# Optimization experiments

Measured on AMD Instinct MI355X. Metric: run time of the kernel, lower is better.

## Reference

```python
import jax, jax.numpy as jnp
import numpy as np

B, STATE_DIM, MLP_DIM, H, W = 128, 64, 512, 40, 40
LN_EPS = 1e-5


def _sobel_kernel(c):
    # Per-channel depthwise filters in torch order: [c0_sx, c0_sy, c0_id, c1_sx, ...]
    sx = jnp.array([[-1., 0., 1.], [-2., 0., 2.], [-1., 0., 1.]], jnp.float32)
    sy = jnp.array([[-1., -2., -1.], [0., 0., 0.], [1., 2., 1.]], jnp.float32)
    ident = jnp.array([[0., 0., 0.], [0., 1., 0.], [0., 0., 0.]], jnp.float32)
    k = jnp.stack([sx, sy, ident])[:, None]      # [3, 1, 3, 3]
    return jnp.tile(k, (c, 1, 1, 1))             # [3c, 1, 3, 3]


def setup_inputs() -> dict:
    key = jax.random.key(0)
    ks = jax.random.split(key, 6)
    state_in = jax.random.normal(ks[0], (B, STATE_DIM, H, W), jnp.float32)
    w1 = jax.random.normal(ks[1], (MLP_DIM, 3 * STATE_DIM), jnp.float32) * 0.05
    ln_weight = jax.random.uniform(ks[2], (MLP_DIM, H, W), jnp.float32, 0.5, 1.5)
    ln_bias = jax.random.normal(ks[3], (MLP_DIM, H, W), jnp.float32) * 0.01
    w2 = jax.random.normal(ks[4], (STATE_DIM, MLP_DIM), jnp.float32) * 0.05
    mask = jax.random.randint(ks[5], (H, W), 0, 2, jnp.int32)  # bernoulli(0.5) update mask
    return {"state_in": state_in, "w1": w1, "ln_weight": ln_weight,
            "ln_bias": ln_bias, "w2": w2, "mask": mask}


def reference(state_in, w1, ln_weight, ln_bias, w2, mask):
    C = state_in.shape[1]
    # Depthwise 3x3 sobel/identity perception: [B, C, H, W] -> [B, 3C, H, W]
    kern = _sobel_kernel(C)
    x = jax.lax.conv_general_dilated(
        state_in, kern, window_strides=(1, 1), padding='SAME',
        dimension_numbers=('NCHW', 'OIHW', 'NCHW'), feature_group_count=C)
    # 1x1 conv (no bias): [B, 3C, H, W] -> [B, MLP, H, W]
    x = jnp.einsum('bchw,oc->bohw', x, w1)
    # LayerNorm over (MLP, H, W) per sample, with elementwise affine
    mu = jnp.mean(x, axis=(1, 2, 3), keepdims=True)
    var = jnp.var(x, axis=(1, 2, 3), keepdims=True)
    x = (x - mu) * jax.lax.rsqrt(var + LN_EPS) * ln_weight + ln_bias
    x = jax.nn.relu(x)
    # 1x1 conv back to state channels (zero-init in original; random here for testing)
    x = jnp.einsum('bchw,oc->bohw', x, w2)
    # Stochastic per-pixel update mask, broadcast over batch and channels
    x = x * mask.astype(jnp.float32)
    # Alive mask: 3x3 max-pool on alive channel, stride 1, SAME padding
    live = jax.lax.reduce_window(state_in[:, 3], -jnp.inf, jax.lax.max,
                                 (1, 3, 3), (1, 1, 1), 'SAME')
    live = (live > 0.1).astype(jnp.float32)[:, None]  # [B, 1, H, W]
    return state_in + x * live
```

## Files before the change

### kernel.cpp

```cpp
#include <hip/hip_runtime.h>


typedef unsigned short u16;
typedef unsigned int   u32;
typedef __attribute__((ext_vector_type(8))) u16    ushort8;
typedef __attribute__((ext_vector_type(4))) u16    u16x4;
typedef __attribute__((ext_vector_type(8))) __bf16 bf16x8;
typedef __attribute__((ext_vector_type(4))) float  f32x4;
typedef __attribute__((ext_vector_type(4))) u32    u32x4;

#define NB   128
#define NC   64
#define K1   192
#define NO   512
#define NHW  1600
#define LN_N 819200.0f

__device__ __forceinline__ u16 f2bf(float f) {
    union { float f; u32 u; } v; v.f = f;
    u32 u = v.u;
    u32 r = u + 0x7fffu + ((u >> 16) & 1u);
    return (u16)(r >> 16);
}
__device__ __forceinline__ float bf2f(u16 h) {
    union { u32 u; float f; } v; v.u = ((u32)h) << 16; return v.f;
}
__device__ __forceinline__ f32x4 mfma16(bf16x8 a, bf16x8 b, f32x4 c) {
    return __builtin_amdgcn_mfma_f32_16x16x32_bf16(a, b, c, 0, 0, 0);
}
__device__ __forceinline__ bf16x8 ldfrag(const u16* p) {
    return *(const bf16x8*)p;
}

__device__ __forceinline__ void load_halo(const float* __restrict__ base, int h,
                                          int wq, float reg[3][12]) {
#pragma unroll
    for (int jj = 0; jj < 3; ++jj) {
        int hh = h + jj - 1;
        bool vh = (unsigned)hh < 40u;
        const float* rowp = base + hh * 40;
#pragma unroll
        for (int i = 0; i < 12; ++i) {
            int col = wq * 10 - 1 + i;
            reg[jj][i] = (vh && (unsigned)col < 40u) ? rowp[col] : 0.0f;
        }
    }
}
__device__ __forceinline__ void sobel_px(const float reg[3][12], int t,
                                         float& sx, float& sy, float& idn) {
    sx = (reg[0][t + 2] - reg[0][t]) + 2.0f * (reg[1][t + 2] - reg[1][t])
       + (reg[2][t + 2] - reg[2][t]);
    sy = (reg[2][t] + 2.0f * reg[2][t + 1] + reg[2][t + 2])
       - (reg[0][t] + 2.0f * reg[0][t + 1] + reg[0][t + 2]);
    idn = reg[1][t + 1];
}

__global__ __launch_bounds__(256) void k0_convert(const float* __restrict__ w1,
                                                  const float* __restrict__ w2,
                                                  u16* __restrict__ w1b,
                                                  u16* __restrict__ w1T,
                                                  u16* __restrict__ w2b,
                                                  float* __restrict__ stats) {
    int g = blockIdx.x * 256 + threadIdx.x;
    if (g < NO * K1) {
        u16 v = f2bf(w1[g]);
        w1b[g] = v;
        int o = g / K1, k = g - o * K1;
        w1T[(size_t)k * NO + o] = v;
    } else if (g < NO * K1 + NC * NO) {
        w2b[g - NO * K1] = f2bf(w2[g - NO * K1]);
    } else if (g < NO * K1 + NC * NO + 256) {
        stats[g - NO * K1 - NC * NO] = 0.0f;
    }
}

__global__ __launch_bounds__(256) void k0_lncomb(const float* __restrict__ lnw,
                                                 const float* __restrict__ lnb,
                                                 u32* __restrict__ lncT) {
    __shared__ u32 t[32][33];
    int p0 = blockIdx.x * 32, o0 = blockIdx.y * 32;
    int tx = threadIdx.x & 31, ty = threadIdx.x >> 5;
#pragma unroll
    for (int k = 0; k < 4; ++k) {
        size_t gi = (size_t)(o0 + ty + k * 8) * NHW + p0 + tx;
        t[ty + k * 8][tx] = ((u32)f2bf(lnb[gi]) << 16) | f2bf(lnw[gi]);
    }
    __syncthreads();
#pragma unroll
    for (int k = 0; k < 4; ++k)
        lncT[(size_t)(p0 + ty + k * 8) * NO + o0 + tx] = t[tx][ty + k * 8];
}

__global__ __launch_bounds__(256) void k0_gram(const u16* __restrict__ w1T,
                                               float* __restrict__ G,
                                               float* __restrict__ colw1) {
    const int blk = blockIdx.x;
    const int tid = threadIdx.x;
    const int lane = tid & 63, wid = tid >> 6;
    const int q = lane >> 4, l15 = lane & 15;
    if (blk < 36) {
        int bj = blk / 6, bk = blk - bj * 6;
        int j0 = bj * 32 + (wid & 1) * 16, k0 = bk * 32 + (wid >> 1) * 16;
        f32x4 acc = {0.f, 0.f, 0.f, 0.f};
#pragma unroll
        for (int ks = 0; ks < 16; ++ks) {
            bf16x8 a  = ldfrag(&w1T[(size_t)(j0 + l15) * NO + ks * 32 + q * 8]);
            bf16x8 bb = ldfrag(&w1T[(size_t)(k0 + l15) * NO + ks * 32 + q * 8]);
            acc = mfma16(a, bb, acc);
        }
#pragma unroll
        for (int r = 0; r < 4; ++r)
            G[(size_t)(j0 + q * 4 + r) * K1 + k0 + l15] = acc[r];
    } else if (tid < K1) {
        float s = 0.f;
        for (int i = 0; i < NO / 8; ++i) {
            ushort8 v = *(const ushort8*)&w1T[(size_t)tid * NO + i * 8];
#pragma unroll
            for (int j = 0; j < 8; ++j) s += bf2f(v[j]);
        }
        colw1[tid] = s;
    }
}

__global__ __launch_bounds__(256) void k2_stats(const float* __restrict__ state,
                                                const float* __restrict__ G,
                                                const float* __restrict__ colw1,
                                                float* __restrict__ stats) {
    const int b = blockIdx.x >> 2, quarter = blockIdx.x & 3;
    const int tid = threadIdx.x;
    const int lane = tid & 63, wid = tid >> 6;
    const int q = lane >> 4, l15 = lane & 15;
    const int j0 = (wid & 1) * 96, j1 = (wid >> 1) * 96, jo = wid * 48;

    __shared__ __align__(16) u16 Pt[208 * 104];
    __shared__ float red[8];

    for (int i = tid; i < 208 * 104 / 2; i += 256) ((u32*)Pt)[i] = 0u;
    __syncthreads();
    if (tid < 80) Pt[192 * 104 + tid] = 0x3F80u;

    f32x4 acc[6][6], accO[3];
#pragma unroll
    for (int i = 0; i < 6; ++i)
#pragma unroll
        for (int j = 0; j < 6; ++j) { f32x4 z = {0.f,0.f,0.f,0.f}; acc[i][j] = z; }
#pragma unroll
    for (int j = 0; j < 3; ++j) { f32x4 z = {0.f,0.f,0.f,0.f}; accO[j] = z; }

    const int c = tid >> 2, wq = tid & 3;
    const float* base = state + ((size_t)b * NC + c) * NHW;

    for (int tile = 0; tile < 5; ++tile) {
        const int h0 = (quarter * 5 + tile) * 2;
        __syncthreads();
        for (int rr = 0; rr < 2; ++rr) {
            float reg[3][12];
            load_halo(base, h0 + rr, wq, reg);
#pragma unroll
            for (int t = 0; t < 10; ++t) {
                float sx, sy, idn; sobel_px(reg, t, sx, sy, idn);
                int px = rr * 40 + wq * 10 + t;
                Pt[(3 * c + 0) * 104 + px] = f2bf(sx);
                Pt[(3 * c + 1) * 104 + px] = f2bf(sy);
                Pt[(3 * c + 2) * 104 + px] = f2bf(idn);
            }
        }
        __syncthreads();
#pragma unroll
        for (int ks = 0; ks < 3; ++ks) {
            bf16x8 av[6], bv[6], ao, bo[3];
#pragma unroll
            for (int fi = 0; fi < 6; ++fi)
                av[fi] = ldfrag(&Pt[(j0 + fi * 16 + l15) * 104 + ks * 32 + q * 8]);
#pragma unroll
            for (int fj = 0; fj < 6; ++fj)
                bv[fj] = ldfrag(&Pt[(j1 + fj * 16 + l15) * 104 + ks * 32 + q * 8]);
            ao = ldfrag(&Pt[(192 + l15) * 104 + ks * 32 + q * 8]);
#pragma unroll
            for (int fj = 0; fj < 3; ++fj)
                bo[fj] = ldfrag(&Pt[(jo + fj * 16 + l15) * 104 + ks * 32 + q * 8]);
#pragma unroll
            for (int fi = 0; fi < 6; ++fi)
#pragma unroll
                for (int fj = 0; fj < 6; ++fj)
                    acc[fi][fj] = mfma16(av[fi], bv[fj], acc[fi][fj]);
#pragma unroll
            for (int fj = 0; fj < 3; ++fj)
                accO[fj] = mfma16(ao, bo[fj], accO[fj]);
        }
    }

    float ssq = 0.f;
#pragma unroll
    for (int fi = 0; fi < 6; ++fi)
#pragma unroll
        for (int fj = 0; fj < 6; ++fj) {
            f32x4 gv = *(const f32x4*)&G[(size_t)(j1 + fj * 16 + l15) * K1
                                         + j0 + fi * 16 + q * 4];
#pragma unroll
            for (int r = 0; r < 4; ++r) ssq += acc[fi][fj][r] * gv[r];
        }
    float sm = 0.f;
    if (q == 0) {
#pragma unroll
        for (int fj = 0; fj < 3; ++fj)
            sm += accO[fj][0] * colw1[jo + fj * 16 + l15];
    }
#pragma unroll
    for (int off = 32; off > 0; off >>= 1) {
        ssq += __shfl_down(ssq, off);
        sm  += __shfl_down(sm, off);
    }
    if (lane == 0) { red[wid] = ssq; red[4 + wid] = sm; }
    __syncthreads();
    if (tid == 0) {
        atomicAdd(&stats[b * 2],     red[4] + red[5] + red[6] + red[7]);
        atomicAdd(&stats[b * 2 + 1], red[0] + red[1] + red[2] + red[3]);
    }
}

__global__ void k3_finalize(const float* __restrict__ stats, float2* __restrict__ musig) {
    int t = threadIdx.x;
    if (t < NB) {
        float s = stats[2 * t], qq = stats[2 * t + 1];
        float inv = 1.0f / LN_N;
        float mu = s * inv;
        float var = qq * inv - mu * mu;
        float2 r; r.x = mu; r.y = rsqrtf(var + 1e-5f);
        musig[t] = r;
    }
}

__global__ __launch_bounds__(256, 3) void k4_fused(const float* __restrict__ state,
                                                   const u16* __restrict__ w1b,
                                                   const u16* __restrict__ w2b,
                                                   const u32* __restrict__ lncT,
                                                   const int* __restrict__ mask,
                                                   const float2* __restrict__ musig,
                                                   float* __restrict__ out) {
    const int bx = blockIdx.x;
    const int b  = blockIdx.y;
    const int p0 = bx * 80, h0 = bx * 2;
    const int tid = threadIdx.x;
    const int lane = tid & 63, wid = tid >> 6;
    const int q = lane >> 4, l15 = lane & 15;

    __shared__ __align__(16) u16 Pt[80 * 192];
    __shared__ __align__(16) u16 Ys[80 * 128];
    __shared__ __align__(16) float gate[80];

    const float2 ms = musig[b];
    const float mu = ms.x, rs = ms.y;

    {
        const int c = tid >> 2, wq = tid & 3;
        const float* base = state + ((size_t)b * NC + c) * NHW;
        for (int rr = 0; rr < 2; ++rr) {
            float reg[3][12];
            load_halo(base, h0 + rr, wq, reg);
#pragma unroll
            for (int t = 0; t < 10; ++t) {
                float sx, sy, idn; sobel_px(reg, t, sx, sy, idn);
                int px = rr * 40 + wq * 10 + t;
                int k = 3 * c;
#pragma unroll
                for (int i = 0; i < 3; ++i) {
                    int kk = k + i, u = kk >> 3;
                    int elem = px * 192 + (((u & 0x18) | ((u ^ px) & 7)) << 3) + (kk & 7);
                    Pt[elem] = f2bf(i == 0 ? sx : (i == 1 ? sy : idn));
                }
            }
        }
    }
    if (tid < 80) {
        int p = p0 + tid;
        int h = p / 40, w = p - h * 40;
        const float* st3 = state + ((size_t)b * NC + 3) * NHW;
        float mx = -1e30f;
#pragma unroll
        for (int dh = -1; dh <= 1; ++dh) {
            int hh = h + dh;
            if ((unsigned)hh < 40u)
#pragma unroll
                for (int dw = -1; dw <= 1; ++dw) {
                    int wc = w + dw;
                    if ((unsigned)wc < 40u) mx = fmaxf(mx, st3[hh * 40 + wc]);
                }
        }
        gate[tid] = (mx > 0.1f && mask[p] != 0) ? 1.0f : 0.0f;
    }
    __syncthreads();

    float g5[5];
#pragma unroll
    for (int mi = 0; mi < 5; ++mi) g5[mi] = gate[mi * 16 + l15];

    f32x4 acc2[5];
#pragma unroll
    for (int i = 0; i < 5; ++i) { f32x4 z = {0.f,0.f,0.f,0.f}; acc2[i] = z; }

    const int ogw = wid * 32;

    for (int oc = 0; oc < 4; ++oc) {
        const int ob = oc * 128 + ogw;
        f32x4 acc1[2][5];
#pragma unroll
        for (int f = 0; f < 2; ++f)
#pragma unroll
            for (int i = 0; i < 5; ++i) { f32x4 z = {0.f,0.f,0.f,0.f}; acc1[f][i] = z; }
#pragma unroll
        for (int ks = 0; ks < 6; ++ks) {
            bf16x8 a0 = ldfrag(&w1b[(size_t)(ob + l15) * K1 + ks * 32 + q * 8]);
            bf16x8 a1 = ldfrag(&w1b[(size_t)(ob + 16 + l15) * K1 + ks * 32 + q * 8]);
#pragma unroll
            for (int mi = 0; mi < 5; ++mi) {
                int r = mi * 16 + l15, u = ks * 4 + q;
                bf16x8 bp = ldfrag(&Pt[r * 192 + (((u & 0x18) | ((u ^ r) & 7)) << 3)]);
                acc1[0][mi] = mfma16(a0, bp, acc1[0][mi]);
                acc1[1][mi] = mfma16(a1, bp, acc1[1][mi]);
            }
        }
#pragma unroll
        for (int f = 0; f < 2; ++f) {
#pragma unroll
            for (int mi = 0; mi < 5; ++mi) {
                int p = mi * 16 + l15;
                int oglob = ob + f * 16 + q * 4;
                u32x4 lv = *(const u32x4*)&lncT[(size_t)(p0 + p) * NO + oglob];
                u16x4 yv;
#pragma unroll
                for (int r = 0; r < 4; ++r) {
                    float lw = bf2f((u16)(lv[r] & 0xffffu));
                    float lb = bf2f((u16)(lv[r] >> 16));
                    float y = (acc1[f][mi][r] - mu) * rs * lw + lb;
                    yv[r] = f2bf(fmaxf(y, 0.0f));
                }
                int u = wid * 4 + f * 2 + (q >> 1);
                int up = u ^ (p & 7);
                *(u16x4*)&Ys[p * 128 + up * 8 + (q & 1) * 4] = yv;
            }
        }
        __syncthreads();
#pragma unroll
        for (int ks2 = 0; ks2 < 4; ++ks2) {
            bf16x8 aw = ldfrag(&w2b[(size_t)(wid * 16 + l15) * NO
                                    + oc * 128 + ks2 * 32 + q * 8]);
#pragma unroll
            for (int mi = 0; mi < 5; ++mi) {
                int p = mi * 16 + l15;
                int u = ks2 * 4 + q;
                int up = u ^ (p & 7);
                bf16x8 by = ldfrag(&Ys[p * 128 + up * 8]);
                acc2[mi] = mfma16(aw, by, acc2[mi]);
            }
        }
        __syncthreads();
    }

#pragma unroll
    for (int mi = 0; mi < 5; ++mi) {
        int p = p0 + mi * 16 + l15;
        float g = g5[mi];
#pragma unroll
        for (int r = 0; r < 4; ++r) {
            int s = wid * 16 + q * 4 + r;
            size_t idx = ((size_t)b * NC + s) * NHW + p;
            out[idx] = state[idx] + g * acc2[mi][r];
        }
    }
}

extern "C" void kernel_launch(void* const* d_in, const int* in_sizes, int n_in,
                              void* d_out, int out_size, void* d_ws, size_t ws_size,
                              hipStream_t stream) {
    const float* state = (const float*)d_in[0];
    const float* w1    = (const float*)d_in[1];
    const float* lnw   = (const float*)d_in[2];
    const float* lnb   = (const float*)d_in[3];
    const float* w2    = (const float*)d_in[4];
    const int*   mask  = (const int*)d_in[5];
    float* out = (float*)d_out;

    char* ws = (char*)d_ws;
    u16*    w1b   = (u16*)(ws + 0ull);
    u16*    w2b   = (u16*)(ws + 196608ull);
    u32*    lncT  = (u32*)(ws + 262144ull);
    u16*    w1T   = (u16*)(ws + 3538944ull);
    float*  G     = (float*)(ws + 3735552ull);
    float*  colw1 = (float*)(ws + 3883008ull);
    float*  stats = (float*)(ws + 3883776ull);
    float2* musig = (float2*)(ws + 3884800ull);

    k0_convert <<<513, 256, 0, stream>>>(w1, w2, w1b, w1T, w2b, stats);
    k0_lncomb  <<<dim3(50, 16), 256, 0, stream>>>(lnw, lnb, lncT);
    k0_gram    <<<37, 256, 0, stream>>>(w1T, G, colw1);
    k2_stats   <<<512, 256, 0, stream>>>(state, G, colw1, stats);
    k3_finalize<<<1, 128, 0, stream>>>(stats, musig);
    k4_fused   <<<dim3(20, 128), 256, 0, stream>>>(state, w1b, w2b, lncT,
                                                   mask, musig, out);
}
```

Before: 337.7 us.

## Prepack weights and LN params in MFMA fragment order, shrink per-iteration tile

Weights w1/w2 and the combined LN weight/bias are rearranged in the setup kernels into the exact per-lane fragment order the fused kernel consumes, so each wave loads them with contiguous vector reads. The output-channel loop now runs 8 chunks of 64 instead of 4 of 128, which halves the accumulator set and the Ys shared buffer so that 4 blocks per CU can be requested. The alive/mask gate is computed per lane in registers instead of through shared memory, and the LN affine is folded into FMAs. The cost is more iterations, which means more barriers per block, plus duplicated max-pool reads in every wave.

```diff
diff --git a/kernel.cpp b/kernel.cpp
--- a/kernel.cpp
+++ b/kernel.cpp
@@ -25,6 +25,12 @@
 __device__ __forceinline__ float bf2f(u16 h) {
     union { u32 u; float f; } v; v.u = ((u32)h) << 16; return v.f;
 }
+__device__ __forceinline__ float bfhi(u32 c) {
+    union { u32 u; float f; } v; v.u = c & 0xffff0000u; return v.f;
+}
+__device__ __forceinline__ float bflo(u32 c) {
+    union { u32 u; float f; } v; v.u = c << 16; return v.f;
+}
 __device__ __forceinline__ f32x4 mfma16(bf16x8 a, bf16x8 b, f32x4 c) {
     return __builtin_amdgcn_mfma_f32_16x16x32_bf16(a, b, c, 0, 0, 0);
 }
@@ -57,18 +63,25 @@
 
 __global__ __launch_bounds__(256) void k0_convert(const float* __restrict__ w1,
                                                   const float* __restrict__ w2,
-                                                  u16* __restrict__ w1b,
+                                                  u16* __restrict__ w1p,
                                                   u16* __restrict__ w1T,
-                                                  u16* __restrict__ w2b,
+                                                  u16* __restrict__ w2p,
                                                   float* __restrict__ stats) {
     int g = blockIdx.x * 256 + threadIdx.x;
     if (g < NO * K1) {
         u16 v = f2bf(w1[g]);
-        w1b[g] = v;
         int o = g / K1, k = g - o * K1;
+        int f = o >> 4, ks = k >> 5;
+        int lane = (((k >> 3) & 3) << 4) | (o & 15);
+        w1p[(size_t)(((f * 6 + ks) * 64 + lane) * 8 + (k & 7))] = v;
         w1T[(size_t)k * NO + o] = v;
     } else if (g < NO * K1 + NC * NO) {
-        w2b[g - NO * K1] = f2bf(w2[g - NO * K1]);
+        int i = g - NO * K1;
+        int s = i / NO, o = i - s * NO;
+        u16 v = f2bf(w2[i]);
+        int wid = s >> 4, oc = o >> 6, ks2 = (o >> 5) & 1;
+        int lane = (((o >> 3) & 3) << 4) | (s & 15);
+        w2p[(size_t)((((wid * 8 + oc) * 2 + ks2) * 64 + lane) * 8 + (o & 7))] = v;
     } else if (g < NO * K1 + NC * NO + 256) {
         stats[g - NO * K1 - NC * NO] = 0.0f;
     }
@@ -76,19 +89,19 @@
 
 __global__ __launch_bounds__(256) void k0_lncomb(const float* __restrict__ lnw,
                                                  const float* __restrict__ lnb,
-                                                 u32* __restrict__ lncT) {
-    __shared__ u32 t[32][33];
-    int p0 = blockIdx.x * 32, o0 = blockIdx.y * 32;
-    int tx = threadIdx.x & 31, ty = threadIdx.x >> 5;
-#pragma unroll
-    for (int k = 0; k < 4; ++k) {
-        size_t gi = (size_t)(o0 + ty + k * 8) * NHW + p0 + tx;
-        t[ty + k * 8][tx] = ((u32)f2bf(lnb[gi]) << 16) | f2bf(lnw[gi]);
-    }
-    __syncthreads();
-#pragma unroll
-    for (int k = 0; k < 4; ++k)
-        lncT[(size_t)(p0 + ty + k * 8) * NO + o0 + tx] = t[tx][ty + k * 8];
+                                                 u32* __restrict__ lnp) {
+    int g = blockIdx.x * 256 + threadIdx.x;
+    int r = g & 3;
+    int lane = (g >> 2) & 63;
+    int rest = g >> 8;
+    int mi = rest % 5;  rest /= 5;
+    int wid = rest & 3; rest >>= 2;
+    int oc = rest & 7;
+    int bx = rest >> 3;
+    int p = bx * 80 + mi * 16 + (lane & 15);
+    int o = oc * 64 + wid * 16 + ((lane >> 4) << 2) + r;
+    size_t gi = (size_t)o * NHW + p;
+    lnp[g] = ((u32)f2bf(lnb[gi]) << 16) | f2bf(lnw[gi]);
 }
 
 __global__ __launch_bounds__(256) void k0_gram(const u16* __restrict__ w1T,
@@ -231,10 +244,10 @@
     }
 }
 
-__global__ __launch_bounds__(256, 3) void k4_fused(const float* __restrict__ state,
-                                                   const u16* __restrict__ w1b,
-                                                   const u16* __restrict__ w2b,
-                                                   const u32* __restrict__ lncT,
+__global__ __launch_bounds__(256, 4) void k4_fused(const float* __restrict__ state,
+                                                   const u16* __restrict__ w1p,
+                                                   const u16* __restrict__ w2p,
+                                                   const u32* __restrict__ lnp,
                                                    const int* __restrict__ mask,
                                                    const float2* __restrict__ musig,
                                                    float* __restrict__ out) {
@@ -246,11 +259,11 @@
     const int q = lane >> 4, l15 = lane & 15;
 
     __shared__ __align__(16) u16 Pt[80 * 192];
-    __shared__ __align__(16) u16 Ys[80 * 128];
-    __shared__ __align__(16) float gate[80];
+    __shared__ __align__(16) u16 Ys[80 * 64];
 
     const float2 ms = musig[b];
     const float mu = ms.x, rs = ms.y;
+    const float murs = mu * rs;
 
     {
         const int c = tid >> 2, wq = tid & 3;
@@ -272,85 +285,84 @@
             }
         }
     }
-    if (tid < 80) {
-        int p = p0 + tid;
-        int h = p / 40, w = p - h * 40;
+    float g5[5];
+    {
         const float* st3 = state + ((size_t)b * NC + 3) * NHW;
-        float mx = -1e30f;
-#pragma unroll
-        for (int dh = -1; dh <= 1; ++dh) {
-            int hh = h + dh;
-            if ((unsigned)hh < 40u)
-#pragma unroll
-                for (int dw = -1; dw <= 1; ++dw) {
-                    int wc = w + dw;
-                    if ((unsigned)wc < 40u) mx = fmaxf(mx, st3[hh * 40 + wc]);
-                }
-        }
-        gate[tid] = (mx > 0.1f && mask[p] != 0) ? 1.0f : 0.0f;
+#pragma unroll
+        for (int mi = 0; mi < 5; ++mi) {
+            int p = p0 + mi * 16 + l15;
+            int h = p / 40, w = p - h * 40;
+            float mx = -1e30f;
+#pragma unroll
+            for (int dh = -1; dh <= 1; ++dh) {
+                int hh = h + dh;
+                if ((unsigned)hh < 40u)
+#pragma unroll
+                    for (int dw = -1; dw <= 1; ++dw) {
+                        int wc = w + dw;
+                        if ((unsigned)wc < 40u) mx = fmaxf(mx, st3[hh * 40 + wc]);
+                    }
+            }
+            g5[mi] = (mx > 0.1f && mask[p] != 0) ? 1.0f : 0.0f;
+        }
     }
     __syncthreads();
 
-    float g5[5];
-#pragma unroll
-    for (int mi = 0; mi < 5; ++mi) g5[mi] = gate[mi * 16 + l15];
-
     f32x4 acc2[5];
 #pragma unroll
     for (int i = 0; i < 5; ++i) { f32x4 z = {0.f,0.f,0.f,0.f}; acc2[i] = z; }
 
-    const int ogw = wid * 32;
-
-    for (int oc = 0; oc < 4; ++oc) {
-        const int ob = oc * 128 + ogw;
-        f32x4 acc1[2][5];
-#pragma unroll
-        for (int f = 0; f < 2; ++f)
-#pragma unroll
-            for (int i = 0; i < 5; ++i) { f32x4 z = {0.f,0.f,0.f,0.f}; acc1[f][i] = z; }
+    for (int oc = 0; oc < 8; ++oc) {
+        u32x4 lv[5];
+        {
+            const u32* lb = lnp + ((((size_t)bx * 8 + oc) * 4 + wid) * 5) * 256 + lane * 4;
+#pragma unroll
+            for (int mi = 0; mi < 5; ++mi)
+                lv[mi] = *(const u32x4*)(lb + mi * 256);
+        }
+        const u16* w2base = w2p + ((size_t)(wid * 8 + oc) * 2) * 512 + lane * 8;
+        bf16x8 aw0 = ldfrag(w2base);
+        bf16x8 aw1 = ldfrag(w2base + 512);
+
+        f32x4 acc1[5];
+#pragma unroll
+        for (int i = 0; i < 5; ++i) { f32x4 z = {0.f,0.f,0.f,0.f}; acc1[i] = z; }
+        const u16* w1base = w1p + ((size_t)(oc * 4 + wid) * 6) * 512 + lane * 8;
 #pragma unroll
         for (int ks = 0; ks < 6; ++ks) {
-            bf16x8 a0 = ldfrag(&w1b[(size_t)(ob + l15) * K1 + ks * 32 + q * 8]);
-            bf16x8 a1 = ldfrag(&w1b[(size_t)(ob + 16 + l15) * K1 + ks * 32 + q * 8]);
+            bf16x8 a = ldfrag(w1base + ks * 512);
 #pragma unroll
             for (int mi = 0; mi < 5; ++mi) {
                 int r = mi * 16 + l15, u = ks * 4 + q;
                 bf16x8 bp = ldfrag(&Pt[r * 192 + (((u & 0x18) | ((u ^ r) & 7)) << 3)]);
-                acc1[0][mi] = mfma16(a0, bp, acc1[0][mi]);
-                acc1[1][mi] = mfma16(a1, bp, acc1[1][mi]);
-            }
-        }
-#pragma unroll
-        for (int f = 0; f < 2; ++f) {
-#pragma unroll
-            for (int mi = 0; mi < 5; ++mi) {
-                int p = mi * 16 + l15;
-                int oglob = ob + f * 16 + q * 4;
-                u32x4 lv = *(const u32x4*)&lncT[(size_t)(p0 + p) * NO + oglob];
-                u16x4 yv;
-#pragma unroll
-                for (int r = 0; r < 4; ++r) {
-                    float lw = bf2f((u16)(lv[r] & 0xffffu));
-                    float lb = bf2f((u16)(lv[r] >> 16));
-                    float y = (acc1[f][mi][r] - mu) * rs * lw + lb;
-                    yv[r] = f2bf(fmaxf(y, 0.0f));
-                }
-                int u = wid * 4 + f * 2 + (q >> 1);
-                int up = u ^ (p & 7);
-                *(u16x4*)&Ys[p * 128 + up * 8 + (q & 1) * 4] = yv;
-            }
+                acc1[mi] = mfma16(a, bp, acc1[mi]);
+            }
+        }
+#pragma unroll
+        for (int mi = 0; mi < 5; ++mi) {
+            int p = mi * 16 + l15;
+            u16x4 yv;
+#pragma unroll
+            for (int r = 0; r < 4; ++r) {
+                u32 cc = lv[mi][r];
+                float t = fmaf(acc1[mi][r], rs, -murs);
+                float y = fmaf(t, bflo(cc), bfhi(cc));
+                yv[r] = f2bf(fmaxf(y, 0.0f));
+            }
+            int u = wid * 2 + (q >> 1);
+            int up = u ^ (p & 7);
+            *(u16x4*)&Ys[p * 64 + up * 8 + (q & 1) * 4] = yv;
         }
         __syncthreads();
 #pragma unroll
-        for (int ks2 = 0; ks2 < 4; ++ks2) {
-            bf16x8 aw = ldfrag(&w2b[(size_t)(wid * 16 + l15) * NO
-                                    + oc * 128 + ks2 * 32 + q * 8]);
+        for (int ks2 = 0; ks2 < 2; ++ks2) {
+            bf16x8 aw = ks2 ? aw1 : aw0;
 #pragma unroll
             for (int mi = 0; mi < 5; ++mi) {
                 int p = mi * 16 + l15;
                 int u = ks2 * 4 + q;
                 int up = u ^ (p & 7);
-                bf16x8 by = ldfrag(&Ys[p * 128 + up * 8]);
+                bf16x8 by = ldfrag(&Ys[p * 64 + up * 8]);
                 acc2[mi] = mfma16(aw, by, acc2[mi]);
             }
         }
@@ -382,20 +394,20 @@
     float* out = (float*)d_out;
 
     char* ws = (char*)d_ws;
-    u16*    w1b   = (u16*)(ws + 0ull);
-    u16*    w2b   = (u16*)(ws + 196608ull);
-    u32*    lncT  = (u32*)(ws + 262144ull);
+    u16*    w1p   = (u16*)(ws + 0ull);
+    u16*    w2p   = (u16*)(ws + 196608ull);
+    u32*    lnp   = (u32*)(ws + 262144ull);
     u16*    w1T   = (u16*)(ws + 3538944ull);
     float*  G     = (float*)(ws + 3735552ull);
     float*  colw1 = (float*)(ws + 3883008ull);
     float*  stats = (float*)(ws + 3883776ull);
     float2* musig = (float2*)(ws + 3884800ull);
 
-    k0_convert <<<513, 256, 0, stream>>>(w1, w2, w1b, w1T, w2b, stats);
-    k0_lncomb  <<<dim3(50, 16), 256, 0, stream>>>(lnw, lnb, lncT);
+    k0_convert <<<513, 256, 0, stream>>>(w1, w2, w1p, w1T, w2p, stats);
+    k0_lncomb  <<<3200, 256, 0, stream>>>(lnw, lnb, lnp);
     k0_gram    <<<37, 256, 0, stream>>>(w1T, G, colw1);
     k2_stats   <<<512, 256, 0, stream>>>(state, G, colw1, stats);
     k3_finalize<<<1, 128, 0, stream>>>(stats, musig);
-    k4_fused   <<<dim3(20, 128), 256, 0, stream>>>(state, w1b, w2b, lncT,
+    k4_fused   <<<dim3(20, 128), 256, 0, stream>>>(state, w1p, w2p, lnp,
                                                    mask, musig, out);
 }
```

New measurement: 300.8 us. -10.9%, faster.
